# Kernel optimization log

Hardware: AMD Instinct MI355X
Metric: run time of the kernel (lower is better)

Reference implementation:

```python
import jax, jax.numpy as jnp
import numpy as np

N = 20000        # nodes
NHID = 128       # hidden channels per head
HEADS = 4
E = 320000       # edges (before self-loops)
NLAYERS = 4
NCLASS = 40
DT, ALPHA, GAMMA = 1.0, 1.0, 1.0
NEG_SLOPE = 0.2  # PyG GATConv default


def setup_inputs() -> dict:
    key = jax.random.key(0)
    ks = jax.random.split(key, 8)
    s = 1.0 / np.sqrt(NHID)
    x = jax.random.normal(ks[0], (N, NHID), jnp.float32)
    src = jax.random.randint(ks[1], (E,), 0, N, dtype=jnp.int32)
    dst = jax.random.randint(ks[2], (E,), 0, N, dtype=jnp.int32)
    W = jax.random.normal(ks[3], (NHID, HEADS * NHID), jnp.float32) * s
    att_src = jax.random.normal(ks[4], (HEADS, NHID), jnp.float32) * s
    att_dst = jax.random.normal(ks[5], (HEADS, NHID), jnp.float32) * s
    bias = jnp.zeros((HEADS * NHID,), jnp.float32)
    Wr = jax.random.normal(ks[6], (NCLASS, NHID), jnp.float32) * s
    br = jnp.zeros((NCLASS,), jnp.float32)
    return {"x": x, "src": src, "dst": dst, "W": W, "att_src": att_src,
            "att_dst": att_dst, "bias": bias, "Wr": Wr, "br": br}


def reference(x, src, dst, W, att_src, att_dst, bias, Wr, br):
    # add self loops (PyG GATConv default)
    loop = jnp.arange(N, dtype=src.dtype)
    s_idx = jnp.concatenate([src, loop])
    d_idx = jnp.concatenate([dst, loop])

    def gat(X):
        # X: [N, NHID] -> out: [N, HEADS*NHID] (head-major, as PyG concat)
        h = (X @ W).reshape(N, HEADS, NHID)                  # [N,H,C]
        a_s = jnp.einsum('nhc,hc->nh', h, att_src)            # [N,H]
        a_d = jnp.einsum('nhc,hc->nh', h, att_dst)            # [N,H]
        e = jax.nn.leaky_relu(a_s[s_idx] + a_d[d_idx], NEG_SLOPE)  # [Etot,H]
        m = jax.ops.segment_max(e, d_idx, num_segments=N)     # scatter-softmax
        ex = jnp.exp(e - m[d_idx])
        den = jax.ops.segment_sum(ex, d_idx, num_segments=N)
        alpha = ex / den[d_idx]                               # [Etot,H]
        msg = h[s_idx] * alpha[..., None]                     # [Etot,H,C]
        out = jax.ops.segment_sum(msg, d_idx, num_segments=N)  # [N,H,C]
        return out.reshape(N, HEADS * NHID) + bias

    def step(carry, _):
        X, Y = carry
        # view(N, -1, nheads).mean(-1) on head-major [N, H*C] layout
        agg = jax.nn.elu(gat(X)).reshape(N, NHID, HEADS).mean(axis=-1)
        Y2 = Y + DT * (agg - ALPHA * Y - GAMMA * X)
        X2 = X + DT * Y2
        return (X2, Y2), (X2, Y2)

    (Xf, Yf), (Xs, Ys) = jax.lax.scan(step, (x, x), None, length=NLAYERS)
    X_all = jnp.concatenate([x[:, None], jnp.moveaxis(Xs, 0, 1)], axis=1)  # [N,L+1,C]
    Y_all = jnp.concatenate([x[:, None], jnp.moveaxis(Ys, 0, 1)], axis=1)
    out = Xf @ Wr.T + br                                     # [N, NCLASS]
    return out, X_all, Y_all
```

## Files before the change

### kernel.cpp

```cpp
#include <hip/hip_runtime.h>

typedef unsigned short u16;
typedef unsigned int u32;

#define N_NODES 20000
#define NE 320000
#define NLAYERS 4
#define NCLASS 40
#define NEG_SLOPE 0.2f
#define LSTRIDE ((NLAYERS + 1) * 128)

typedef __bf16 bf16x8 __attribute__((ext_vector_type(8)));
typedef float f32x4 __attribute__((ext_vector_type(4)));

__device__ inline u16 f2bf(float f) {
    u32 u = __float_as_uint(f);
    return (u16)((u + 0x7fffu + ((u >> 16) & 1u)) >> 16);
}
__device__ inline u32 pack2bf(float lo, float hi) {
    return (u32)f2bf(lo) | ((u32)f2bf(hi) << 16);
}

#define P1_INIT 10000
#define P1_TRANS 256
#define P1_FOLD 128
#define P1_COUNT 1250
__global__ __launch_bounds__(256) void k_pre1(
    const float* __restrict__ x, const int* __restrict__ dst,
    const float* __restrict__ W, const float* __restrict__ att_s,
    const float* __restrict__ att_d,
    u16* __restrict__ Xbf, float* __restrict__ Xall, float* __restrict__ Yall,
    u16* __restrict__ Wt, float* __restrict__ Vs, float* __restrict__ Vd,
    int* __restrict__ counts) {
    int b = blockIdx.x;
    if (b < P1_INIT) {
        int t = b * 256 + threadIdx.x;
        float v = x[t];
        Xbf[t] = f2bf(v);
        int n = t >> 7, c = t & 127;
        int ob = n * LSTRIDE + c;
        Xall[ob] = v;
        Yall[ob] = v;
    } else if (b < P1_INIT + P1_TRANS) {
        int t = (b - P1_INIT) * 256 + threadIdx.x;
        int k = t >> 9, col = t & 511;
        Wt[col * 128 + k] = f2bf(W[t]);
    } else if (b < P1_INIT + P1_TRANS + P1_FOLD) {
        int wid = ((b - P1_INIT - P1_TRANS) * 256 + threadIdx.x) >> 6;
        int lane = threadIdx.x & 63;
        int t = wid >> 2, hd = wid & 3;
        float w0 = W[t * 512 + hd * 128 + lane];
        float w1 = W[t * 512 + hd * 128 + 64 + lane];
        float s1 = w0 * att_s[hd * 128 + lane] + w1 * att_s[hd * 128 + 64 + lane];
        float s2 = w0 * att_d[hd * 128 + lane] + w1 * att_d[hd * 128 + 64 + lane];
        for (int off = 32; off; off >>= 1) {
            s1 += __shfl_xor(s1, off);
            s2 += __shfl_xor(s2, off);
        }
        if (lane == 0) {
            Vs[t * 4 + hd] = s1;
            Vd[t * 4 + hd] = s2;
        }
    } else {
        int t = (b - P1_INIT - P1_TRANS - P1_FOLD) * 256 + threadIdx.x;
        atomicAdd(&counts[dst[t]], 1);
    }
}

__global__ __launch_bounds__(1024) void k_pre2(
    const int* __restrict__ counts, int* __restrict__ indptr, int* __restrict__ cursor,
    const float* __restrict__ x, const float* __restrict__ Vs, const float* __restrict__ Vd,
    float* __restrict__ a_s, float* __restrict__ a_d) {
    if (blockIdx.x == 0) {
        __shared__ int part[1024];
        int t = threadIdx.x;
        const int CH = 20;
        int c0 = t * CH;
        int s = 0;
        for (int i = 0; i < CH; i++) {
            int idx = c0 + i;
            if (idx < N_NODES) s += counts[idx] + 1;
        }
        part[t] = s;
        __syncthreads();
        for (int off = 1; off < 1024; off <<= 1) {
            int v = 0;
            if (t >= off) v = part[t - off];
            __syncthreads();
            if (t >= off) part[t] += v;
            __syncthreads();
        }
        int ex = (t == 0) ? 0 : part[t - 1];
        for (int i = 0; i < CH; i++) {
            int idx = c0 + i;
            if (idx < N_NODES) {
                indptr[idx] = ex;
                cursor[idx] = ex;
                ex += counts[idx] + 1;
            }
        }
        if (t == 1023) indptr[N_NODES] = part[1023];
    } else {
        int wave = threadIdx.x >> 6, lane = threadIdx.x & 63;
        int n = (blockIdx.x - 1) * 16 + wave;
        const float* Xr = x + n * 128;
        float x0 = Xr[lane], x1 = Xr[64 + lane];
        f32x4 vs0 = *(const f32x4*)(Vs + lane * 4), vs1 = *(const f32x4*)(Vs + (64 + lane) * 4);
        f32x4 vd0 = *(const f32x4*)(Vd + lane * 4), vd1 = *(const f32x4*)(Vd + (64 + lane) * 4);
        f32x4 ps = x0 * vs0 + x1 * vs1;
        f32x4 pd = x0 * vd0 + x1 * vd1;
        for (int off = 32; off; off >>= 1)
            for (int c = 0; c < 4; c++) {
                ps[c] += __shfl_xor(ps[c], off);
                pd[c] += __shfl_xor(pd[c], off);
            }
        if (lane == 0) {
            *(f32x4*)(a_s + n * 4) = ps;
            *(f32x4*)(a_d + n * 4) = pd;
        }
    }
}

__global__ void k_scatter(const int* __restrict__ src, const int* __restrict__ dst,
                          int* __restrict__ cursor, int* __restrict__ esrc) {
    int t = blockIdx.x * 256 + threadIdx.x;
    if (t >= NE + N_NODES) return;
    int s, d;
    if (t < NE) { s = src[t]; d = dst[t]; }
    else { s = d = t - NE; }
    int pos = atomicAdd(&cursor[d], 1);
    esrc[pos] = s;
}

__global__ __launch_bounds__(512) void k_layer(
    const int* __restrict__ indptr, const int* __restrict__ esrc,
    const float* __restrict__ a_s, const float* __restrict__ a_d,
    const u16* __restrict__ XbfR, const u16* __restrict__ Wt,
    const float* __restrict__ bias,
    float* __restrict__ Xall, float* __restrict__ Yall, u16* __restrict__ XbfW,
    float* __restrict__ a_s_nxt, float* __restrict__ a_d_nxt,
    const float* __restrict__ Vs, const float* __restrict__ Vd,
    int layer, int do_logits) {
    __shared__ int s_sh[8][2][66];
    __shared__ alignas(16) float al_sh[8][2][66][4];
    __shared__ u16 As[16 * 520];
    __shared__ float aggbuf[16 * 130];
    const int t = threadIdx.x;
    const int r0 = blockIdx.x * 16;
    const int w = t >> 6, lane = t & 63;

    f32x4 acc00 = {0.f, 0.f, 0.f, 0.f}, acc01 = {0.f, 0.f, 0.f, 0.f};
    f32x4 acc10 = {0.f, 0.f, 0.f, 0.f}, acc11 = {0.f, 0.f, 0.f, 0.f};
    int d0 = r0 + w * 2;
    int st0 = indptr[d0], en0 = indptr[d0 + 1], en1 = indptr[d0 + 2];
    int st1 = en0;
    int deg0 = en0 - st0, deg1 = en1 - st1;
    f32x4 ad0 = *(const f32x4*)(a_d + d0 * 4);
    f32x4 ad1 = *(const f32x4*)(a_d + d0 * 4 + 4);

    auto prep = [&](int nd, int st, int en, f32x4 ad) {
        int j = st + lane;
        int s = 0;
        f32x4 e = {-1e30f, -1e30f, -1e30f, -1e30f};
        if (j < en) {
            s = esrc[j];
            f32x4 as = *(const f32x4*)(a_s + s * 4);
            for (int c = 0; c < 4; c++) {
                float v = as[c] + ad[c];
                e[c] = v > 0.f ? v : NEG_SLOPE * v;
            }
        }
        f32x4 mx = e;
        for (int off = 32; off; off >>= 1)
            for (int c = 0; c < 4; c++) mx[c] = fmaxf(mx[c], __shfl_xor(mx[c], off));
        f32x4 p;
        for (int c = 0; c < 4; c++) p[c] = __expf(e[c] - mx[c]);
        f32x4 den = p;
        for (int off = 32; off; off >>= 1)
            for (int c = 0; c < 4; c++) den[c] += __shfl_xor(den[c], off);
        f32x4 alpha;
        for (int c = 0; c < 4; c++) alpha[c] = p[c] * (1.f / den[c]);
        s_sh[w][nd][lane] = s;
        *(f32x4*)al_sh[w][nd][lane] = alpha;
        if (lane == 63) {
            s_sh[w][nd][64] = 0;
            f32x4 z = {0.f, 0.f, 0.f, 0.f};
            *(f32x4*)al_sh[w][nd][64] = z;
        }
    };
    auto chunk1 = [&](int nd, int cnt, f32x4& aL, f32x4& aH) {
        int sc = s_sh[w][nd][0];
        f32x4 al = *(const f32x4*)al_sh[w][nd][0];
        u32 xv = *(const u32*)(XbfR + sc * 128 + lane * 2);
        for (int i = 0; i < cnt; i++) {
            int sn = s_sh[w][nd][i + 1];
            f32x4 an = *(const f32x4*)al_sh[w][nd][i + 1];
            u32 xn = *(const u32*)(XbfR + sn * 128 + lane * 2);
            aL += al * __uint_as_float(xv << 16);
            aH += al * __uint_as_float(xv & 0xffff0000u);
            xv = xn;
            al = an;
        }
    };
    auto gen = [&](int nd, int st, int en, f32x4 ad, f32x4& aL, f32x4& aH) {
        f32x4 mx = {-1e30f, -1e30f, -1e30f, -1e30f};
        for (int j = st + lane; j < en; j += 64) {
            int s = esrc[j];
            f32x4 e = *(const f32x4*)(a_s + s * 4) + ad;
            for (int c = 0; c < 4; c++) {
                float v = e[c];
                v = v > 0.f ? v : NEG_SLOPE * v;
                mx[c] = fmaxf(mx[c], v);
            }
        }
        for (int off = 32; off; off >>= 1)
            for (int c = 0; c < 4; c++) mx[c] = fmaxf(mx[c], __shfl_xor(mx[c], off));
        f32x4 den = {0.f, 0.f, 0.f, 0.f};
        for (int j = st + lane; j < en; j += 64) {
            int s = esrc[j];
            f32x4 e = *(const f32x4*)(a_s + s * 4) + ad;
            for (int c = 0; c < 4; c++) {
                float v = e[c];
                v = v > 0.f ? v : NEG_SLOPE * v;
                den[c] += __expf(v - mx[c]);
            }
        }
        for (int off = 32; off; off >>= 1)
            for (int c = 0; c < 4; c++) den[c] += __shfl_xor(den[c], off);
        f32x4 rd;
        for (int c = 0; c < 4; c++) rd[c] = 1.f / den[c];
        for (int base = st; base < en; base += 64) {
            int cnt = min(64, en - base);
            int jj = base + lane;
            int s = 0;
            f32x4 alpha = {0.f, 0.f, 0.f, 0.f};
            if (jj < en) {
                s = esrc[jj];
                f32x4 e = *(const f32x4*)(a_s + s * 4) + ad;
                for (int c = 0; c < 4; c++) {
                    float v = e[c];
                    v = v > 0.f ? v : NEG_SLOPE * v;
                    alpha[c] = __expf(v - mx[c]) * rd[c];
                }
            }
            s_sh[w][nd][lane] = s;
            *(f32x4*)al_sh[w][nd][lane] = alpha;
            if (lane == 63) {
                s_sh[w][nd][64] = 0;
                f32x4 z = {0.f, 0.f, 0.f, 0.f};
                *(f32x4*)al_sh[w][nd][64] = z;
            }
            __builtin_amdgcn_wave_barrier();
            chunk1(nd, cnt, aL, aH);
            __builtin_amdgcn_wave_barrier();
        }
    };

    if (deg0 <= 64 && deg1 <= 64) {
        prep(0, st0, en0, ad0);
        prep(1, st1, en1, ad1);
        __builtin_amdgcn_wave_barrier();
        int cm = deg0 > deg1 ? deg0 : deg1;
        int sA = s_sh[w][0][0], sB = s_sh[w][1][0];
        f32x4 aA = *(const f32x4*)al_sh[w][0][0];
        f32x4 aB = *(const f32x4*)al_sh[w][1][0];
        u32 xA = *(const u32*)(XbfR + sA * 128 + lane * 2);
        u32 xB = *(const u32*)(XbfR + sB * 128 + lane * 2);
        for (int i = 0; i < cm; i++) {
            int sA2 = s_sh[w][0][i + 1], sB2 = s_sh[w][1][i + 1];
            f32x4 aA2 = *(const f32x4*)al_sh[w][0][i + 1];
            f32x4 aB2 = *(const f32x4*)al_sh[w][1][i + 1];
            u32 xA2 = *(const u32*)(XbfR + sA2 * 128 + lane * 2);
            u32 xB2 = *(const u32*)(XbfR + sB2 * 128 + lane * 2);
            acc00 += aA * __uint_as_float(xA << 16);
            acc01 += aA * __uint_as_float(xA & 0xffff0000u);
            acc10 += aB * __uint_as_float(xB << 16);
            acc11 += aB * __uint_as_float(xB & 0xffff0000u);
            xA = xA2; aA = aA2; xB = xB2; aB = aB2;
        }
    } else {
        gen(0, st0, en0, ad0, acc00, acc01);
        gen(1, st1, en1, ad1, acc10, acc11);
    }

    {
        u16* a0 = As + (w * 2) * 520 + lane * 2;
        u16* a1 = As + (w * 2 + 1) * 520 + lane * 2;
        for (int h = 0; h < 4; h++) {
            *(u32*)(a0 + h * 128) = pack2bf(acc00[h], acc01[h]);
            *(u32*)(a1 + h * 128) = pack2bf(acc10[h], acc11[h]);
        }
    }
    __syncthreads();

    const int h = w >> 1, colhalf = w & 1;
    const int lrow = lane & 15, quad = lane >> 4;
    f32x4 macc[4] = {};
    for (int k4 = 0; k4 < 4; k4++) {
        bf16x8 a = *(const bf16x8*)(As + lrow * 520 + h * 128 + k4 * 32 + quad * 8);
        for (int ni = 0; ni < 4; ni++) {
            bf16x8 bfrag = *(const bf16x8*)(Wt + (h * 128 + colhalf * 64 + ni * 16 + lrow) * 128 +
                                            k4 * 32 + quad * 8);
            macc[ni] = __builtin_amdgcn_mfma_f32_16x16x32_bf16(a, bfrag, macc[ni], 0, 0, 0);
        }
    }
    for (int ni = 0; ni < 4; ni++) {
        float bv = bias[h * 128 + colhalf * 64 + ni * 16 + lrow];
        for (int r = 0; r < 4; r++) {
            float v = macc[ni][r] + bv;
            v = v > 0.f ? v : __expf(v) - 1.f;
            v += __shfl_xor(v, 1);
            v += __shfl_xor(v, 2);
            if ((lrow & 3) == 0) {
                int row = quad * 4 + r;
                int cO = h * 32 + colhalf * 16 + ni * 4 + (lrow >> 2);
                aggbuf[row * 130 + cO] = 0.25f * v;
            }
        }
    }
    __syncthreads();

    {
        int c = t & 127, rg = t >> 7;
        for (int rr = 0; rr < 4; rr++) {
            int row = rg * 4 + rr;
            float agg = aggbuf[row * 130 + c];
            int node = r0 + row;
            int xo = node * LSTRIDE + layer * 128 + c;
            float xp = Xall[xo];
            Xall[xo + 128] = agg;
            Yall[xo + 128] = agg - xp;
            XbfW[node * 128 + c] = f2bf(agg);
        }
    }
    if (do_logits) {
        f32x4 vs0 = *(const f32x4*)(Vs + lane * 4), vs1 = *(const f32x4*)(Vs + (64 + lane) * 4);
        f32x4 vd0 = *(const f32x4*)(Vd + lane * 4), vd1 = *(const f32x4*)(Vd + (64 + lane) * 4);
        for (int rr = 0; rr < 2; rr++) {
            int row = w * 2 + rr;
            float x0 = aggbuf[row * 130 + lane], x1 = aggbuf[row * 130 + 64 + lane];
            f32x4 ps = x0 * vs0 + x1 * vs1;
            f32x4 pd = x0 * vd0 + x1 * vd1;
            for (int off = 32; off; off >>= 1)
                for (int c2 = 0; c2 < 4; c2++) {
                    ps[c2] += __shfl_xor(ps[c2], off);
                    pd[c2] += __shfl_xor(pd[c2], off);
                }
            if (lane == 0) {
                int node = r0 + row;
                *(f32x4*)(a_s_nxt + node * 4) = ps;
                *(f32x4*)(a_d_nxt + node * 4) = pd;
            }
        }
    }
}

__global__ __launch_bounds__(256) void k_out(const float* __restrict__ Xall,
                                             const float* __restrict__ Wr,
                                             const float* __restrict__ br,
                                             float* __restrict__ out) {
    __shared__ float Xs[4][128];
    int wave = threadIdx.x >> 6, lane = threadIdx.x & 63;
    int n = blockIdx.x * 4 + wave;
    const float* Xr = Xall + n * LSTRIDE + NLAYERS * 128;
    Xs[wave][lane] = Xr[lane];
    Xs[wave][64 + lane] = Xr[64 + lane];
    __syncthreads();
    if (lane < NCLASS) {
        float acc = 0.f;
        for (int kc = 0; kc < 32; kc++) {
            f32x4 wv = *(const f32x4*)(Wr + lane * 128 + kc * 4);
            for (int q = 0; q < 4; q++) acc += Xs[wave][kc * 4 + q] * wv[q];
        }
        out[n * NCLASS + lane] = acc + br[lane];
    }
}

extern "C" void kernel_launch(void* const* d_in, const int* in_sizes, int n_in,
                              void* d_out, int out_size, void* d_ws, size_t ws_size,
                              hipStream_t stream) {
    const float* x = (const float*)d_in[0];
    const int* src = (const int*)d_in[1];
    const int* dst = (const int*)d_in[2];
    const float* W = (const float*)d_in[3];
    const float* att_s = (const float*)d_in[4];
    const float* att_d = (const float*)d_in[5];
    const float* bias = (const float*)d_in[6];
    const float* Wr = (const float*)d_in[7];
    const float* br = (const float*)d_in[8];

    float* out = (float*)d_out;
    float* Xall = out + (size_t)N_NODES * NCLASS;
    float* Yall = Xall + (size_t)N_NODES * LSTRIDE;

    char* p = (char*)d_ws;
    auto alloc = [&](size_t bytes) -> char* {
        char* r = p;
        p += (bytes + 255) & ~(size_t)255;
        return r;
    };
    u16* XbfA = (u16*)alloc((size_t)N_NODES * 128 * 2);
    u16* XbfB = (u16*)alloc((size_t)N_NODES * 128 * 2);
    u16* Wt = (u16*)alloc(512 * 128 * 2);
    float* a_sA = (float*)alloc((size_t)N_NODES * 4 * 4);
    float* a_dA = (float*)alloc((size_t)N_NODES * 4 * 4);
    float* a_sB = (float*)alloc((size_t)N_NODES * 4 * 4);
    float* a_dB = (float*)alloc((size_t)N_NODES * 4 * 4);
    float* Vs = (float*)alloc(128 * 4 * 4);
    float* Vd = (float*)alloc(128 * 4 * 4);
    int* indptr = (int*)alloc((N_NODES + 1) * 4);
    int* cursor = (int*)alloc(N_NODES * 4);
    int* counts = (int*)alloc(N_NODES * 4);
    int* esrc = (int*)alloc((size_t)(NE + N_NODES) * 4);

    hipMemsetAsync(counts, 0, N_NODES * sizeof(int), stream);
    k_pre1<<<P1_INIT + P1_TRANS + P1_FOLD + P1_COUNT, 256, 0, stream>>>(
        x, dst, W, att_s, att_d, XbfA, Xall, Yall, Wt, Vs, Vd, counts);
    k_pre2<<<1251, 1024, 0, stream>>>(counts, indptr, cursor, x, Vs, Vd, a_sA, a_dA);
    k_scatter<<<(NE + N_NODES + 255) / 256, 256, 0, stream>>>(src, dst, cursor, esrc);

    for (int layer = 0; layer < NLAYERS; layer++) {
        const float* as_r = (layer & 1) ? a_sB : a_sA;
        const float* ad_r = (layer & 1) ? a_dB : a_dA;
        float* as_w = (layer & 1) ? a_sA : a_sB;
        float* ad_w = (layer & 1) ? a_dA : a_dB;
        const u16* xr = (layer & 1) ? XbfB : XbfA;
        u16* xw = (layer & 1) ? XbfA : XbfB;
        k_layer<<<N_NODES / 16, 512, 0, stream>>>(indptr, esrc, as_r, ad_r, xr, Wt, bias,
                                                  Xall, Yall, xw, as_w, ad_w, Vs, Vd, layer,
                                                  (layer + 1 < NLAYERS) ? 1 : 0);
    }
    k_out<<<N_NODES / 4, 256, 0, stream>>>(Xall, Wr, br, out);
}
```

Measured before the change: 478.1 us.

## Gather four edges per wave with wide loads, shrink blocks, fuse output projection

The layer kernel now uses 256-thread blocks covering 8 nodes instead of 512 threads covering 16. Each wave in the low-degree path processes four edges at once, using 16-byte bf16 row loads and cross-lane shuffles to reduce the per-head partial sums. The MFMA stage is reorganized so each wave computes one full head, and the final classifier matmul is folded into the last layer launch, removing the separate output kernel. The aim is better memory-level parallelism and occupancy in the gather and one fewer launch. The cost is more registers for the per-lane accumulators and MFMA work on 8 padding rows that are discarded.

```diff
diff --git a/kernel.cpp b/kernel.cpp
--- a/kernel.cpp
+++ b/kernel.cpp
@@ -132,7 +132,7 @@
     esrc[pos] = s;
 }
 
-__global__ __launch_bounds__(512) void k_layer(
+__global__ __launch_bounds__(256, 5) void k_layer(
     const int* __restrict__ indptr, const int* __restrict__ esrc,
     const float* __restrict__ a_s, const float* __restrict__ a_d,
     const u16* __restrict__ XbfR, const u16* __restrict__ Wt,
@@ -140,17 +140,17 @@
     float* __restrict__ Xall, float* __restrict__ Yall, u16* __restrict__ XbfW,
     float* __restrict__ a_s_nxt, float* __restrict__ a_d_nxt,
     const float* __restrict__ Vs, const float* __restrict__ Vd,
-    int layer, int do_logits) {
-    __shared__ int s_sh[8][2][66];
-    __shared__ alignas(16) float al_sh[8][2][66][4];
-    __shared__ u16 As[16 * 520];
-    __shared__ float aggbuf[16 * 130];
+    const float* __restrict__ Wr, const float* __restrict__ br, float* __restrict__ outp,
+    int layer, int mode) {
+    __shared__ int s_sh[4][2][72];
+    __shared__ alignas(16) float al_sh[4][2][72][4];
+    __shared__ alignas(16) u16 As[16 * 520];
+    __shared__ float aggbuf[8 * 132];
     const int t = threadIdx.x;
-    const int r0 = blockIdx.x * 16;
+    const int r0 = blockIdx.x * 8;
     const int w = t >> 6, lane = t & 63;
-
-    f32x4 acc00 = {0.f, 0.f, 0.f, 0.f}, acc01 = {0.f, 0.f, 0.f, 0.f};
-    f32x4 acc10 = {0.f, 0.f, 0.f, 0.f}, acc11 = {0.f, 0.f, 0.f, 0.f};
+    const int g = lane >> 4, c = lane & 15;
+
     int d0 = r0 + w * 2;
     int st0 = indptr[d0], en0 = indptr[d0 + 1], en1 = indptr[d0 + 2];
     int st1 = en0;
@@ -165,29 +165,71 @@
         if (j < en) {
             s = esrc[j];
             f32x4 as = *(const f32x4*)(a_s + s * 4);
-            for (int c = 0; c < 4; c++) {
-                float v = as[c] + ad[c];
-                e[c] = v > 0.f ? v : NEG_SLOPE * v;
+            for (int cc = 0; cc < 4; cc++) {
+                float v = as[cc] + ad[cc];
+                e[cc] = v > 0.f ? v : NEG_SLOPE * v;
             }
         }
         f32x4 mx = e;
         for (int off = 32; off; off >>= 1)
-            for (int c = 0; c < 4; c++) mx[c] = fmaxf(mx[c], __shfl_xor(mx[c], off));
+            for (int cc = 0; cc < 4; cc++) mx[cc] = fmaxf(mx[cc], __shfl_xor(mx[cc], off));
         f32x4 p;
-        for (int c = 0; c < 4; c++) p[c] = __expf(e[c] - mx[c]);
+        for (int cc = 0; cc < 4; cc++) p[cc] = __expf(e[cc] - mx[cc]);
         f32x4 den = p;
         for (int off = 32; off; off >>= 1)
-            for (int c = 0; c < 4; c++) den[c] += __shfl_xor(den[c], off);
+            for (int cc = 0; cc < 4; cc++) den[cc] += __shfl_xor(den[cc], off);
         f32x4 alpha;
-        for (int c = 0; c < 4; c++) alpha[c] = p[c] * (1.f / den[c]);
+        for (int cc = 0; cc < 4; cc++) alpha[cc] = p[cc] * (1.f / den[cc]);
         s_sh[w][nd][lane] = s;
         *(f32x4*)al_sh[w][nd][lane] = alpha;
-        if (lane == 63) {
-            s_sh[w][nd][64] = 0;
+        if (lane >= 60) {
+            s_sh[w][nd][lane + 4] = 0;
             f32x4 z = {0.f, 0.f, 0.f, 0.f};
-            *(f32x4*)al_sh[w][nd][64] = z;
+            *(f32x4*)al_sh[w][nd][lane + 4] = z;
         }
     };
+
+    auto gather4 = [&](int nd, int st, int deg, int row) {
+        float pacc[4][8] = {};
+        int ni = (deg + 3) >> 2;
+        int e = g;
+        int s0 = s_sh[w][nd][e];
+        f32x4 al = *(const f32x4*)al_sh[w][nd][e];
+        uint4 xv = *(const uint4*)(XbfR + s0 * 128 + c * 8);
+        for (int i = 0; i < ni; i++) {
+            int e1 = e + 4;
+            int s1 = s_sh[w][nd][e1];
+            f32x4 al1 = *(const f32x4*)al_sh[w][nd][e1];
+            uint4 xn = *(const uint4*)(XbfR + s1 * 128 + c * 8);
+            u32 uu[4] = {xv.x, xv.y, xv.z, xv.w};
+            float xf[8];
+            for (int m = 0; m < 4; m++) {
+                xf[2 * m] = __uint_as_float(uu[m] << 16);
+                xf[2 * m + 1] = __uint_as_float(uu[m] & 0xffff0000u);
+            }
+            for (int h = 0; h < 4; h++)
+                for (int k = 0; k < 8; k++)
+                    pacc[h][k] += al[h] * xf[k];
+            xv = xn; al = al1; e = e1;
+        }
+        bool hi2 = (g & 2) != 0, hi1 = (g & 1) != 0;
+        float F[8];
+        for (int k = 0; k < 8; k++) {
+            float kA = hi2 ? pacc[2][k] : pacc[0][k];
+            float sA = hi2 ? pacc[0][k] : pacc[2][k];
+            float t0 = kA + __shfl_xor(sA, 32);
+            float kB = hi2 ? pacc[3][k] : pacc[1][k];
+            float sB = hi2 ? pacc[1][k] : pacc[3][k];
+            float t1 = kB + __shfl_xor(sB, 32);
+            float kC = hi1 ? t1 : t0;
+            float sC = hi1 ? t0 : t1;
+            F[k] = kC + __shfl_xor(sC, 16);
+        }
+        *(uint4*)(As + row * 520 + g * 128 + c * 8) =
+            make_uint4(pack2bf(F[0], F[1]), pack2bf(F[2], F[3]),
+                       pack2bf(F[4], F[5]), pack2bf(F[6], F[7]));
+    };
+
     auto chunk1 = [&](int nd, int cnt, f32x4& aL, f32x4& aH) {
         int sc = s_sh[w][nd][0];
         f32x4 al = *(const f32x4*)al_sh[w][nd][0];
@@ -198,37 +240,37 @@
             u32 xn = *(const u32*)(XbfR + sn * 128 + lane * 2);
             aL += al * __uint_as_float(xv << 16);
             aH += al * __uint_as_float(xv & 0xffff0000u);
-            xv = xn;
-            al = an;
+            xv = xn; al = an;
         }
     };
-    auto gen = [&](int nd, int st, int en, f32x4 ad, f32x4& aL, f32x4& aH) {
+    auto gen = [&](int nd, int st, int en, f32x4 ad, int row) {
+        f32x4 accL = {0.f, 0.f, 0.f, 0.f}, accH = {0.f, 0.f, 0.f, 0.f};
         f32x4 mx = {-1e30f, -1e30f, -1e30f, -1e30f};
         for (int j = st + lane; j < en; j += 64) {
             int s = esrc[j];
             f32x4 e = *(const f32x4*)(a_s + s * 4) + ad;
-            for (int c = 0; c < 4; c++) {
-                float v = e[c];
+            for (int cc = 0; cc < 4; cc++) {
+                float v = e[cc];
                 v = v > 0.f ? v : NEG_SLOPE * v;
-                mx[c] = fmaxf(mx[c], v);
+                mx[cc] = fmaxf(mx[cc], v);
             }
         }
         for (int off = 32; off; off >>= 1)
-            for (int c = 0; c < 4; c++) mx[c] = fmaxf(mx[c], __shfl_xor(mx[c], off));
+            for (int cc = 0; cc < 4; cc++) mx[cc] = fmaxf(mx[cc], __shfl_xor(mx[cc], off));
         f32x4 den = {0.f, 0.f, 0.f, 0.f};
         for (int j = st + lane; j < en; j += 64) {
             int s = esrc[j];
             f32x4 e = *(const f32x4*)(a_s + s * 4) + ad;
-            for (int c = 0; c < 4; c++) {
-                float v = e[c];
+            for (int cc = 0; cc < 4; cc++) {
+                float v = e[cc];
                 v = v > 0.f ? v : NEG_SLOPE * v;
-                den[c] += __expf(v - mx[c]);
+                den[cc] += __expf(v - mx[cc]);
             }
         }
         for (int off = 32; off; off >>= 1)
-            for (int c = 0; c < 4; c++) den[c] += __shfl_xor(den[c], off);
+            for (int cc = 0; cc < 4; cc++) den[cc] += __shfl_xor(den[cc], off);
         f32x4 rd;
-        for (int c = 0; c < 4; c++) rd[c] = 1.f / den[c];
+        for (int cc = 0; cc < 4; cc++) rd[cc] = 1.f / den[cc];
         for (int base = st; base < en; base += 64) {
             int cnt = min(64, en - base);
             int jj = base + lane;
@@ -237,10 +279,10 @@
             if (jj < en) {
                 s = esrc[jj];
                 f32x4 e = *(const f32x4*)(a_s + s * 4) + ad;
-                for (int c = 0; c < 4; c++) {
-                    float v = e[c];
+                for (int cc = 0; cc < 4; cc++) {
+                    float v = e[cc];
                     v = v > 0.f ? v : NEG_SLOPE * v;
-                    alpha[c] = __expf(v - mx[c]) * rd[c];
+                    alpha[cc] = __expf(v - mx[cc]) * rd[cc];
                 }
             }
             s_sh[w][nd][lane] = s;
@@ -251,94 +293,63 @@
                 *(f32x4*)al_sh[w][nd][64] = z;
             }
             __builtin_amdgcn_wave_barrier();
-            chunk1(nd, cnt, aL, aH);
+            chunk1(nd, cnt, accL, accH);
             __builtin_amdgcn_wave_barrier();
         }
+        u16* a0 = As + row * 520 + lane * 2;
+        for (int h = 0; h < 4; h++)
+            *(u32*)(a0 + h * 128) = pack2bf(accL[h], accH[h]);
     };
 
-    if (deg0 <= 64 && deg1 <= 64) {
-        prep(0, st0, en0, ad0);
-        prep(1, st1, en1, ad1);
-        __builtin_amdgcn_wave_barrier();
-        int cm = deg0 > deg1 ? deg0 : deg1;
-        int sA = s_sh[w][0][0], sB = s_sh[w][1][0];
-        f32x4 aA = *(const f32x4*)al_sh[w][0][0];
-        f32x4 aB = *(const f32x4*)al_sh[w][1][0];
-        u32 xA = *(const u32*)(XbfR + sA * 128 + lane * 2);
-        u32 xB = *(const u32*)(XbfR + sB * 128 + lane * 2);
-        for (int i = 0; i < cm; i++) {
-            int sA2 = s_sh[w][0][i + 1], sB2 = s_sh[w][1][i + 1];
-            f32x4 aA2 = *(const f32x4*)al_sh[w][0][i + 1];
-            f32x4 aB2 = *(const f32x4*)al_sh[w][1][i + 1];
-            u32 xA2 = *(const u32*)(XbfR + sA2 * 128 + lane * 2);
-            u32 xB2 = *(const u32*)(XbfR + sB2 * 128 + lane * 2);
-            acc00 += aA * __uint_as_float(xA << 16);
-            acc01 += aA * __uint_as_float(xA & 0xffff0000u);
-            acc10 += aB * __uint_as_float(xB << 16);
-            acc11 += aB * __uint_as_float(xB & 0xffff0000u);
-            xA = xA2; aA = aA2; xB = xB2; aB = aB2;
-        }
-    } else {
-        gen(0, st0, en0, ad0, acc00, acc01);
-        gen(1, st1, en1, ad1, acc10, acc11);
-    }
-
-    {
-        u16* a0 = As + (w * 2) * 520 + lane * 2;
-        u16* a1 = As + (w * 2 + 1) * 520 + lane * 2;
-        for (int h = 0; h < 4; h++) {
-            *(u32*)(a0 + h * 128) = pack2bf(acc00[h], acc01[h]);
-            *(u32*)(a1 + h * 128) = pack2bf(acc10[h], acc11[h]);
-        }
-    }
+    prep(0, st0, en0, ad0);
+    prep(1, st1, en1, ad1);
+    __builtin_amdgcn_wave_barrier();
+    if (deg0 <= 64) gather4(0, st0, deg0, w * 2); else gen(0, st0, en0, ad0, w * 2);
+    if (deg1 <= 64) gather4(1, st1, deg1, w * 2 + 1); else gen(1, st1, en1, ad1, w * 2 + 1);
     __syncthreads();
 
-    const int h = w >> 1, colhalf = w & 1;
-    const int lrow = lane & 15, quad = lane >> 4;
-    f32x4 macc[4] = {};
+    f32x4 macc[8] = {};
     for (int k4 = 0; k4 < 4; k4++) {
-        bf16x8 a = *(const bf16x8*)(As + lrow * 520 + h * 128 + k4 * 32 + quad * 8);
-        for (int ni = 0; ni < 4; ni++) {
-            bf16x8 bfrag = *(const bf16x8*)(Wt + (h * 128 + colhalf * 64 + ni * 16 + lrow) * 128 +
-                                            k4 * 32 + quad * 8);
+        bf16x8 a = *(const bf16x8*)(As + c * 520 + w * 128 + k4 * 32 + g * 8);
+        for (int ni = 0; ni < 8; ni++) {
+            bf16x8 bfrag = *(const bf16x8*)(Wt + (w * 128 + ni * 16 + c) * 128 + k4 * 32 + g * 8);
             macc[ni] = __builtin_amdgcn_mfma_f32_16x16x32_bf16(a, bfrag, macc[ni], 0, 0, 0);
         }
     }
-    for (int ni = 0; ni < 4; ni++) {
-        float bv = bias[h * 128 + colhalf * 64 + ni * 16 + lrow];
+    for (int ni = 0; ni < 8; ni++) {
+        float bv = bias[w * 128 + ni * 16 + c];
         for (int r = 0; r < 4; r++) {
             float v = macc[ni][r] + bv;
             v = v > 0.f ? v : __expf(v) - 1.f;
             v += __shfl_xor(v, 1);
             v += __shfl_xor(v, 2);
-            if ((lrow & 3) == 0) {
-                int row = quad * 4 + r;
-                int cO = h * 32 + colhalf * 16 + ni * 4 + (lrow >> 2);
-                aggbuf[row * 130 + cO] = 0.25f * v;
+            if ((c & 3) == 0 && g < 2) {
+                int row = g * 4 + r;
+                aggbuf[row * 132 + w * 32 + ni * 4 + (c >> 2)] = 0.25f * v;
             }
         }
     }
     __syncthreads();
 
     {
-        int c = t & 127, rg = t >> 7;
+        int c2 = t & 127, rg = t >> 7;
         for (int rr = 0; rr < 4; rr++) {
             int row = rg * 4 + rr;
-            float agg = aggbuf[row * 130 + c];
+            float agg = aggbuf[row * 132 + c2];
             int node = r0 + row;
-            int xo = node * LSTRIDE + layer * 128 + c;
+            int xo = node * LSTRIDE + layer * 128 + c2;
             float xp = Xall[xo];
             Xall[xo + 128] = agg;
             Yall[xo + 128] = agg - xp;
-            XbfW[node * 128 + c] = f2bf(agg);
-        }
-    }
-    if (do_logits) {
+            XbfW[node * 128 + c2] = f2bf(agg);
+        }
+    }
+    if (mode == 0) {
         f32x4 vs0 = *(const f32x4*)(Vs + lane * 4), vs1 = *(const f32x4*)(Vs + (64 + lane) * 4);
         f32x4 vd0 = *(const f32x4*)(Vd + lane * 4), vd1 = *(const f32x4*)(Vd + (64 + lane) * 4);
         for (int rr = 0; rr < 2; rr++) {
             int row = w * 2 + rr;
-            float x0 = aggbuf[row * 130 + lane], x1 = aggbuf[row * 130 + 64 + lane];
+            float x0 = aggbuf[row * 132 + lane], x1 = aggbuf[row * 132 + 64 + lane];
             f32x4 ps = x0 * vs0 + x1 * vs1;
             f32x4 pd = x0 * vd0 + x1 * vd1;
             for (int off = 32; off; off >>= 1)
@@ -352,27 +363,19 @@
                 *(f32x4*)(a_d_nxt + node * 4) = pd;
             }
         }
-    }
-}
-
-__global__ __launch_bounds__(256) void k_out(const float* __restrict__ Xall,
-                                             const float* __restrict__ Wr,
-                                             const float* __restrict__ br,
-                                             float* __restrict__ out) {
-    __shared__ float Xs[4][128];
-    int wave = threadIdx.x >> 6, lane = threadIdx.x & 63;
-    int n = blockIdx.x * 4 + wave;
-    const float* Xr = Xall + n * LSTRIDE + NLAYERS * 128;
-    Xs[wave][lane] = Xr[lane];
-    Xs[wave][64 + lane] = Xr[64 + lane];
-    __syncthreads();
-    if (lane < NCLASS) {
-        float acc = 0.f;
-        for (int kc = 0; kc < 32; kc++) {
-            f32x4 wv = *(const f32x4*)(Wr + lane * 128 + kc * 4);
-            for (int q = 0; q < 4; q++) acc += Xs[wave][kc * 4 + q] * wv[q];
-        }
-        out[n * NCLASS + lane] = acc + br[lane];
+    } else {
+        if (lane < NCLASS) {
+            for (int rr = 0; rr < 2; rr++) {
+                int row = w * 2 + rr;
+                float accv = 0.f;
+                for (int kc = 0; kc < 32; kc++) {
+                    f32x4 wv = *(const f32x4*)(Wr + lane * 128 + kc * 4);
+                    f32x4 xv = *(const f32x4*)&aggbuf[row * 132 + kc * 4];
+                    accv += wv[0] * xv[0] + wv[1] * xv[1] + wv[2] * xv[2] + wv[3] * xv[3];
+                }
+                outp[(r0 + row) * NCLASS + lane] = accv + br[lane];
+            }
+        }
     }
 }
 
@@ -426,9 +429,9 @@
         float* ad_w = (layer & 1) ? a_dA : a_dB;
         const u16* xr = (layer & 1) ? XbfB : XbfA;
         u16* xw = (layer & 1) ? XbfA : XbfB;
-        k_layer<<<N_NODES / 16, 512, 0, stream>>>(indptr, esrc, as_r, ad_r, xr, Wt, bias,
-                                                  Xall, Yall, xw, as_w, ad_w, Vs, Vd, layer,
-                                                  (layer + 1 < NLAYERS) ? 1 : 0);
-    }
-    k_out<<<N_NODES / 4, 256, 0, stream>>>(Xall, Wr, br, out);
-}
+        k_layer<<<N_NODES / 8, 256, 0, stream>>>(indptr, esrc, as_r, ad_r, xr, Wt, bias,
+                                                 Xall, Yall, xw, as_w, ad_w, Vs, Vd,
+                                                 Wr, br, out, layer,
+                                                 (layer + 1 < NLAYERS) ? 0 : 1);
+    }
+}
```

Measured after the change: 586.9 us. 1.23x slower.
